# Performance work log

Measured on AMD Instinct MI355X. Metric: run time of the kernel, lower is better.

Reference implementation:

```python
import jax, jax.numpy as jnp
import numpy as np

B, L, D, H = 4, 4096, 2048, 128


def setup_inputs() -> dict:
    key = jax.random.key(0)
    k1, k2, k3, k4 = jax.random.split(key, 4)
    scale = 1.0 / np.sqrt(D)
    return {
        "x": jax.random.normal(k1, (B, L, D), dtype=jnp.float32),
        "Wq": jax.random.normal(k2, (D, H), dtype=jnp.float32) * scale,
        "Wk": jax.random.normal(k3, (D, H), dtype=jnp.float32) * scale,
        "Wv": jax.random.normal(k4, (D, H), dtype=jnp.float32) * scale,
    }


def reference(x, Wq, Wk, Wv):
    # single-head causal self-attention (dropout in eval mode / p=0)
    L_ = x.shape[1]
    q = jnp.einsum("bld,dh->blh", x, Wq)  # [B,L,H]
    k = jnp.einsum("bld,dh->blh", x, Wk)
    v = jnp.einsum("bld,dh->blh", x, Wv)
    scores = jnp.einsum("bqh,bkh->bqk", q, k) / jnp.sqrt(jnp.float32(q.shape[-1]))
    causal = jnp.tril(jnp.ones((L_, L_), dtype=bool))
    scores = jnp.where(causal, scores, -jnp.inf)
    probs = jax.nn.softmax(scores, axis=-1)
    return jnp.einsum("bqk,bkh->bqh", probs, v)
```

## Files before the change

kernel.cpp:

```cpp
#include <hip/hip_runtime.h>
#include <hip/hip_bf16.h>

#define B_ 4
#define L_ 4096
#define D_ 2048
#define H_ 128
#define M_ (B_ * L_)

typedef __attribute__((ext_vector_type(8))) short bf16x8;
typedef __attribute__((ext_vector_type(4))) float f32x4;
typedef __attribute__((ext_vector_type(16))) float f32x16;

__device__ __forceinline__ unsigned short f2bf(float f) {
  union { float f; unsigned u; } v; v.f = f;
  unsigned r = v.u + 0x7FFFu + ((v.u >> 16) & 1u);
  return (unsigned short)(r >> 16);
}

__device__ __forceinline__ unsigned cvt_pk_bf16(float lo, float hi) {
  unsigned r;
  asm("v_cvt_pk_bf16_f32 %0, %1, %2" : "=v"(r) : "v"(lo), "v"(hi));
  return r;
}

__device__ __forceinline__ void async_copy16(void* lds, const void* gptr) {
  __builtin_amdgcn_global_load_lds(
      (const __attribute__((address_space(1))) unsigned int*)gptr,
      (__attribute__((address_space(3))) unsigned int*)lds, 16, 0, 0);
}

__global__ void wconv(const float* __restrict__ Wq, const float* __restrict__ Wk,
                      const float* __restrict__ Wv, unsigned short* __restrict__ Wt) {
  int i = blockIdx.x * 256 + threadIdx.x;
  int m = i >> 18;
  int rem = i & 262143;
  int n = rem >> 11;
  int d = rem & 2047;
  const float* W = (m == 0) ? Wq : (m == 1 ? Wk : Wv);
  float val = W[(size_t)d * H_ + n];
  if (m == 0) val *= 0.08838834764831845f;
  int R = 96 * (n >> 5) + 32 * m + (n & 31);
  Wt[(size_t)R * D_ + d] = f2bf(val);
}

__global__ __launch_bounds__(512, 1) void qkv_gemm(
    const float* __restrict__ x, const unsigned short* __restrict__ Wt,
    unsigned short* __restrict__ qo, unsigned short* __restrict__ ko,
    unsigned short* __restrict__ vt) {
  __shared__ __align__(16) char Ab[2][16384];
  __shared__ __align__(16) char Bb[2][49152];

  int tid = threadIdx.x;
  int row0 = blockIdx.x * 64;
  int lane = tid & 63, w = tid >> 6;
  int wrow = (w >> 2) * 32;
  int g = w & 3;
  int l15 = lane & 15, lhi = lane >> 4;

  f32x4 zero = {0.f, 0.f, 0.f, 0.f};
  f32x4 acc[2][6];
#pragma unroll
  for (int i = 0; i < 2; i++)
#pragma unroll
    for (int j = 0; j < 6; j++) acc[i][j] = zero;

  const char* xg = (const char*)x;
  const char* wg = (const char*)Wt;

#pragma unroll
  for (int p = 0; p < 2; p++) {
    int o = (p * 512 + tid) * 16;
    int r = o >> 8;
    int cb = (o & 255) ^ ((r & 7) << 4);
    async_copy16(Ab[0] + o, xg + (((size_t)(row0 + r) * D_) << 2) + cb);
  }
#pragma unroll
  for (int p = 0; p < 6; p++) {
    int o = (p * 512 + tid) * 16;
    int r = o >> 7;
    int cb = (o & 127) ^ ((r & 7) << 4);
    async_copy16(Bb[0] + o, wg + (((size_t)r * D_) << 1) + cb);
  }
  __syncthreads();

  for (int t = 0; t < 32; t++) {
    int buf = t & 1;
    if (t < 31) {
      int k0 = (t + 1) * 64;
#pragma unroll
      for (int p = 0; p < 2; p++) {
        int o = (p * 512 + tid) * 16;
        int r = o >> 8;
        int cb = (o & 255) ^ ((r & 7) << 4);
        async_copy16(Ab[buf ^ 1] + o, xg + (((size_t)(row0 + r) * D_ + k0) << 2) + cb);
      }
#pragma unroll
      for (int p = 0; p < 6; p++) {
        int o = (p * 512 + tid) * 16;
        int r = o >> 7;
        int cb = (o & 127) ^ ((r & 7) << 4);
        async_copy16(Bb[buf ^ 1] + o, wg + (((size_t)r * D_ + k0) << 1) + cb);
      }
    }
    const char* A = Ab[buf];
    const char* Bp = Bb[buf];
#pragma unroll
    for (int ks = 0; ks < 2; ks++) {
      bf16x8 af[2], bfr[6];
#pragma unroll
      for (int mi = 0; mi < 2; mi++) {
        int r = wrow + mi * 16 + l15;
        int sw = (r & 7) << 4;
        int cb = ks * 128 + lhi * 32;
        float4 lo = *(const float4*)(A + r * 256 + (cb ^ sw));
        float4 hi = *(const float4*)(A + r * 256 + ((cb + 16) ^ sw));
        union { bf16x8 v; unsigned u[4]; } tt;
        tt.u[0] = cvt_pk_bf16(lo.x, lo.y);
        tt.u[1] = cvt_pk_bf16(lo.z, lo.w);
        tt.u[2] = cvt_pk_bf16(hi.x, hi.y);
        tt.u[3] = cvt_pk_bf16(hi.z, hi.w);
        af[mi] = tt.v;
      }
#pragma unroll
      for (int ni = 0; ni < 6; ni++) {
        int r = g * 96 + ni * 16 + l15;
        int sw = (r & 7) << 4;
        int cb = ks * 64 + lhi * 16;
        bfr[ni] = *(const bf16x8*)(Bp + r * 128 + (cb ^ sw));
      }
#pragma unroll
      for (int mi = 0; mi < 2; mi++)
#pragma unroll
        for (int ni = 0; ni < 6; ni++)
          acc[mi][ni] = __builtin_amdgcn_mfma_f32_16x16x32_bf16(af[mi], bfr[ni], acc[mi][ni], 0, 0, 0);
    }
    __syncthreads();
  }

#pragma unroll
  for (int ni = 0; ni < 4; ni++) {
    unsigned short* dst = (ni < 2) ? qo : ko;
    int nn = 32 * g + (ni & 1) * 16 + l15;
#pragma unroll
    for (int mi = 0; mi < 2; mi++)
#pragma unroll
      for (int r = 0; r < 4; r++) {
        int m = row0 + wrow + mi * 16 + lhi * 4 + r;
        dst[(size_t)m * H_ + nn] = f2bf(acc[mi][ni][r]);
      }
  }
  unsigned short* Tls = (unsigned short*)(Bb[0]) + w * 1280;
#pragma unroll
  for (int ni = 4; ni < 6; ni++)
#pragma unroll
    for (int mi = 0; mi < 2; mi++)
#pragma unroll
      for (int r = 0; r < 4; r++)
        Tls[((ni - 4) * 16 + l15) * 40 + mi * 16 + lhi * 4 + r] = f2bf(acc[mi][ni][r]);
  {
    int b = row0 >> 12;
    int Lbase = (row0 & 4095) + wrow;
    int n_loc = lane >> 1;
    int half = (lane & 1) * 16;
    int h = 32 * g + n_loc;
#pragma unroll
    for (int j = 0; j < 2; j++) {
      bf16x8 v = *(const bf16x8*)&Tls[n_loc * 40 + half + j * 8];
      *(bf16x8*)&vt[(((size_t)(b * H_ + h)) << 12) + Lbase + half + j * 8] = v;
    }
  }
}

__global__ __launch_bounds__(256, 2) void attn(
    const unsigned short* __restrict__ q, const unsigned short* __restrict__ k,
    const unsigned short* __restrict__ vt, float* __restrict__ po,
    float* __restrict__ pm, float* __restrict__ pl) {
  __shared__ __align__(16) char Kb[2][16384];
  __shared__ __align__(16) char Vb[2][16384];

  int bid = blockIdx.x;
  int b = bid & 3;
  int p2 = bid >> 2;
  int j, c;
  if (p2 < 32)      { j = 31 - (p2 >> 2);            c = p2 & 3; }
  else if (p2 < 56) { int i = p2 - 32; int d3 = i / 3; j = 23 - d3; c = i - 3 * d3; }
  else if (p2 < 72) { int i = p2 - 56; j = 15 - (i >> 1); c = i & 1; }
  else              { j = 7 - (p2 - 72);             c = 0; }

  int kbase = c << 10;
  int kmax = min((c + 1) << 10, (j + 1) << 7);
  int NT = (kmax - kbase) >> 6;

  int tid = threadIdx.x;
  int w = tid >> 6, lane = tid & 63;
  int q31 = lane & 31, hi = lane >> 5;
  int qw0 = (j << 7) + (w << 5);
  int kcap = qw0 + 32;

  const unsigned short* qb = q + ((size_t)b << 12) * H_;
  const char* kbyte = (const char*)(k + ((size_t)b << 12) * H_);
  const char* vbyte = (const char*)(vt + ((size_t)b * H_ << 12));

  bf16x8 qf[8];
#pragma unroll
  for (int kk = 0; kk < 8; kk++)
    qf[kk] = *(const bf16x8*)&qb[(size_t)(qw0 + q31) * H_ + kk * 16 + hi * 8];

  f32x16 o[4];
#pragma unroll
  for (int hb = 0; hb < 4; hb++)
#pragma unroll
    for (int r = 0; r < 16; r++) o[hb][r] = 0.f;
  float mrun = -1e30f, lrun = 0.f;

  int ksw = (q31 & 7) << 4;

#define STAGE(bi, k0)                                                          \
  {                                                                            \
    _Pragma("unroll") for (int p = 0; p < 4; p++) {                            \
      int oo = (p * 256 + tid) * 16;                                           \
      int rr = oo >> 8;                                                        \
      int cc = (oo & 255) ^ ((rr & 7) << 4);                                   \
      async_copy16(Kb[bi] + oo, kbyte + (size_t)((k0) + rr) * 256 + cc);       \
    }                                                                          \
    _Pragma("unroll") for (int p = 0; p < 4; p++) {                            \
      int oo = (p * 256 + tid) * 16;                                           \
      int hh = oo >> 7;                                                        \
      int cc = (oo & 127) ^ ((hh & 7) << 4);                                   \
      async_copy16(Vb[bi] + oo, vbyte + (size_t)hh * 8192 + (size_t)(k0) * 2 + cc); \
    }                                                                          \
  }

  STAGE(0, kbase);

  for (int t = 0; t < NT; t++) {
    __syncthreads();
    int k0 = kbase + (t << 6);
    if (t + 1 < NT) STAGE((t + 1) & 1, k0 + 64);
    const char* Kc = Kb[t & 1];
    const char* Vc = Vb[t & 1];

#pragma unroll
    for (int sub = 0; sub < 2; sub++) {
      int k0s = k0 + (sub << 5);
      if (k0s < kcap) {
        int kloc2 = sub << 5;
        const char* Krow = Kc + (kloc2 + q31) * 256;
        f32x16 s;
#pragma unroll
        for (int r = 0; r < 16; r++) s[r] = 0.f;
#pragma unroll
        for (int kk = 0; kk < 8; kk++) {
          bf16x8 kf = *(const bf16x8*)(Krow + ((kk * 32 + hi * 16) ^ ksw));
          s = __builtin_amdgcn_mfma_f32_32x32x16_bf16(kf, qf[kk], s, 0, 0, 0);
        }
        if (k0s == qw0) {
#pragma unroll
          for (int r = 0; r < 16; r++) {
            int kloc = (r & 3) + 8 * (r >> 2) + 4 * hi;
            if (kloc > q31) s[r] = -1e30f;
          }
        }
        float m0 = fmaxf(fmaxf(s[0], s[1]), fmaxf(s[2], s[3]));
        float m1 = fmaxf(fmaxf(s[4], s[5]), fmaxf(s[6], s[7]));
        float m2 = fmaxf(fmaxf(s[8], s[9]), fmaxf(s[10], s[11]));
        float m3 = fmaxf(fmaxf(s[12], s[13]), fmaxf(s[14], s[15]));
        float mt = fmaxf(fmaxf(m0, m1), fmaxf(m2, m3));
        mt = fmaxf(mt, __shfl_xor(mt, 32, 64));
        if (!__all(mt <= mrun + 8.f)) {
          float mn = fmaxf(mrun, mt);
          float al = __expf(mrun - mn);
          mrun = mn;
          lrun *= al;
#pragma unroll
          for (int hb = 0; hb < 4; hb++)
#pragma unroll
            for (int r = 0; r < 16; r++) o[hb][r] *= al;
        }
        float p[16], ls = 0.f;
#pragma unroll
        for (int r = 0; r < 16; r++) {
          p[r] = __expf(s[r] - mrun);
          ls += p[r];
        }
        ls += __shfl_xor(ls, 32, 64);
        lrun += ls;
        unsigned c0 = cvt_pk_bf16(p[0], p[1]),   c1 = cvt_pk_bf16(p[2], p[3]);
        unsigned c2 = cvt_pk_bf16(p[4], p[5]),   c3 = cvt_pk_bf16(p[6], p[7]);
        unsigned c4 = cvt_pk_bf16(p[8], p[9]),   c5 = cvt_pk_bf16(p[10], p[11]);
        unsigned c6 = cvt_pk_bf16(p[12], p[13]), c7 = cvt_pk_bf16(p[14], p[15]);
        unsigned e0 = (unsigned)__shfl_xor((int)(hi ? c0 : c2), 32, 64);
        unsigned e1 = (unsigned)__shfl_xor((int)(hi ? c1 : c3), 32, 64);
        unsigned e2 = (unsigned)__shfl_xor((int)(hi ? c4 : c6), 32, 64);
        unsigned e3 = (unsigned)__shfl_xor((int)(hi ? c5 : c7), 32, 64);
        union { unsigned u[4]; bf16x8 v; } pb0, pb1;
        pb0.u[0] = hi ? e0 : c0; pb0.u[1] = hi ? e1 : c1;
        pb0.u[2] = hi ? c2 : e0; pb0.u[3] = hi ? c3 : e1;
        pb1.u[0] = hi ? e2 : c4; pb1.u[1] = hi ? e3 : c5;
        pb1.u[2] = hi ? c6 : e2; pb1.u[3] = hi ? c7 : e3;
#pragma unroll
        for (int hb = 0; hb < 4; hb++) {
          const char* Vrow = Vc + (hb * 32 + q31) * 128;
          bf16x8 v0 = *(const bf16x8*)(Vrow + ((kloc2 * 2 + hi * 16) ^ ksw));
          bf16x8 v1 = *(const bf16x8*)(Vrow + ((kloc2 * 2 + 32 + hi * 16) ^ ksw));
          o[hb] = __builtin_amdgcn_mfma_f32_32x32x16_bf16(v0, pb0.v, o[hb], 0, 0, 0);
          o[hb] = __builtin_amdgcn_mfma_f32_32x32x16_bf16(v1, pb1.v, o[hb], 0, 0, 0);
        }
      }
    }
  }
#undef STAGE

  int qtile = (j << 2) + w;
  int slot = (((b << 7) + qtile) << 2) + c;
  float* pob = po + ((size_t)slot << 12);
#pragma unroll
  for (int hb = 0; hb < 4; hb++)
#pragma unroll
    for (int rq = 0; rq < 4; rq++) {
      float4 v;
      v.x = o[hb][rq * 4 + 0];
      v.y = o[hb][rq * 4 + 1];
      v.z = o[hb][rq * 4 + 2];
      v.w = o[hb][rq * 4 + 3];
      *(float4*)&pob[q31 * 128 + 32 * hb + 8 * rq + 4 * hi] = v;
    }
  if (lane < 32) {
    pm[slot * 32 + q31] = mrun;
    pl[slot * 32 + q31] = lrun;
  }
}

__global__ __launch_bounds__(256) void combine(
    const float* __restrict__ po, const float* __restrict__ pm,
    const float* __restrict__ pl, float* __restrict__ out) {
  int bid = blockIdx.x;
  int b = bid >> 7, t = bid & 127;
  int nc = (((t + 1) << 5) + 1023) >> 10;
  int tid = threadIdx.x;
  int row = tid >> 3;
  int hb = (tid & 7) << 4;
  int base = bid * 4;

  float M = -1e30f;
  for (int ci = 0; ci < nc; ci++) M = fmaxf(M, pm[(base + ci) * 32 + row]);
  float L = 0.f;
  float a[16];
#pragma unroll
  for (int j = 0; j < 16; j++) a[j] = 0.f;
  for (int ci = 0; ci < nc; ci++) {
    int sl = base + ci;
    float wgt = __expf(pm[sl * 32 + row] - M);
    L += pl[sl * 32 + row] * wgt;
    const float* p = po + ((size_t)sl << 12) + row * 128 + hb;
#pragma unroll
    for (int j = 0; j < 4; j++) {
      float4 v = *(const float4*)(p + j * 4);
      a[j * 4 + 0] += v.x * wgt;
      a[j * 4 + 1] += v.y * wgt;
      a[j * 4 + 2] += v.z * wgt;
      a[j * 4 + 3] += v.w * wgt;
    }
  }
  float inv = 1.f / L;
  float* ob = out + ((size_t)((b << 12) + (t << 5) + row)) * 128 + hb;
#pragma unroll
  for (int j = 0; j < 16; j++) ob[j] = a[j] * inv;
}

extern "C" void kernel_launch(void* const* d_in, const int* in_sizes, int n_in,
                              void* d_out, int out_size, void* d_ws, size_t ws_size,
                              hipStream_t stream) {
  const float* x  = (const float*)d_in[0];
  const float* Wq = (const float*)d_in[1];
  const float* Wk = (const float*)d_in[2];
  const float* Wv = (const float*)d_in[3];

  unsigned short* ws = (unsigned short*)d_ws;
  unsigned short* Wt = ws;
  unsigned short* qo = ws + 786432;
  unsigned short* ko = qo + (size_t)M_ * H_;
  unsigned short* vt = ko + (size_t)M_ * H_;
  float* po = (float*)(vt + (size_t)M_ * H_);
  float* pm = po + (size_t)2048 * 4096;
  float* pl = pm + 2048 * 32;
  float* out = (float*)d_out;

  hipLaunchKernelGGL(wconv, dim3(3072), dim3(256), 0, stream, Wq, Wk, Wv, Wt);
  hipLaunchKernelGGL(qkv_gemm, dim3(256), dim3(512), 0, stream, x, Wt, qo, ko, vt);
  hipLaunchKernelGGL(attn, dim3(320), dim3(256), 0, stream, qo, ko, vt, po, pm, pl);
  hipLaunchKernelGGL(combine, dim3(512), dim3(256), 0, stream, po, pm, pl, out);
}
```

Baseline: 286.9 us.

## Halve QKV GEMM k-tile to fit more blocks per CU with explicit vmcnt waits

The QKV projection GEMM's k-step shrinks from 64 to 32, halving its LDS double buffers, and launch bounds go from 1 to 4 blocks per CU so more workgroups can be resident. The __syncthreads at the top of each iteration becomes an explicit s_waitcnt vmcnt(4) plus s_barrier, so the next stage's async copies can stay in flight while the current buffer is consumed. The cost is twice as many iterations and barriers, smaller swizzle patterns, and register pressure under the tighter launch bound.

```diff
diff --git a/kernel.cpp b/kernel.cpp
--- a/kernel.cpp
+++ b/kernel.cpp
@@ -43,12 +43,12 @@
   Wt[(size_t)R * D_ + d] = f2bf(val);
 }
 
-__global__ __launch_bounds__(512, 1) void qkv_gemm(
+__global__ __launch_bounds__(512, 4) void qkv_gemm(
     const float* __restrict__ x, const unsigned short* __restrict__ Wt,
     unsigned short* __restrict__ qo, unsigned short* __restrict__ ko,
     unsigned short* __restrict__ vt) {
-  __shared__ __align__(16) char Ab[2][16384];
-  __shared__ __align__(16) char Bb[2][49152];
+  __shared__ __align__(16) char Ab[2][8192];
+  __shared__ __align__(16) char Bb[2][24576];
 
   int tid = threadIdx.x;
   int row0 = blockIdx.x * 64;
@@ -67,75 +67,68 @@
   const char* xg = (const char*)x;
   const char* wg = (const char*)Wt;
 
-#pragma unroll
-  for (int p = 0; p < 2; p++) {
-    int o = (p * 512 + tid) * 16;
-    int r = o >> 8;
-    int cb = (o & 255) ^ ((r & 7) << 4);
-    async_copy16(Ab[0] + o, xg + (((size_t)(row0 + r) * D_) << 2) + cb);
-  }
-#pragma unroll
-  for (int p = 0; p < 6; p++) {
-    int o = (p * 512 + tid) * 16;
-    int r = o >> 7;
-    int cb = (o & 127) ^ ((r & 7) << 4);
-    async_copy16(Bb[0] + o, wg + (((size_t)r * D_) << 1) + cb);
-  }
-  __syncthreads();
-
-  for (int t = 0; t < 32; t++) {
+#define QSTAGE(bi, k0)                                                         \
+  {                                                                            \
+    {                                                                          \
+      int o = tid * 16;                                                        \
+      int r = o >> 7;                                                          \
+      int cb = (o & 127) ^ ((r & 7) << 4);                                     \
+      async_copy16(Ab[bi] + o, xg + (((size_t)(row0 + r) * D_ + (k0)) << 2) + cb); \
+    }                                                                          \
+    _Pragma("unroll") for (int p = 0; p < 3; p++) {                            \
+      int o = (p * 512 + tid) * 16;                                            \
+      int r = o >> 6;                                                          \
+      int cb = (o & 63) ^ ((r & 3) << 4);                                      \
+      async_copy16(Bb[bi] + o, wg + (((size_t)r * D_ + (k0)) << 1) + cb);      \
+    }                                                                          \
+  }
+
+  QSTAGE(0, 0);
+
+  for (int t = 0; t < 64; t++) {
     int buf = t & 1;
-    if (t < 31) {
-      int k0 = (t + 1) * 64;
-#pragma unroll
-      for (int p = 0; p < 2; p++) {
-        int o = (p * 512 + tid) * 16;
-        int r = o >> 8;
-        int cb = (o & 255) ^ ((r & 7) << 4);
-        async_copy16(Ab[buf ^ 1] + o, xg + (((size_t)(row0 + r) * D_ + k0) << 2) + cb);
-      }
-#pragma unroll
-      for (int p = 0; p < 6; p++) {
-        int o = (p * 512 + tid) * 16;
-        int r = o >> 7;
-        int cb = (o & 127) ^ ((r & 7) << 4);
-        async_copy16(Bb[buf ^ 1] + o, wg + (((size_t)r * D_ + k0) << 1) + cb);
-      }
-    }
+    if (t < 63) {
+      QSTAGE(buf ^ 1, (t + 1) * 32);
+      asm volatile("s_waitcnt vmcnt(4)" ::: "memory");
+    } else {
+      asm volatile("s_waitcnt vmcnt(0)" ::: "memory");
+    }
+    __builtin_amdgcn_s_barrier();
+
     const char* A = Ab[buf];
     const char* Bp = Bb[buf];
-#pragma unroll
-    for (int ks = 0; ks < 2; ks++) {
-      bf16x8 af[2], bfr[6];
-#pragma unroll
-      for (int mi = 0; mi < 2; mi++) {
-        int r = wrow + mi * 16 + l15;
-        int sw = (r & 7) << 4;
-        int cb = ks * 128 + lhi * 32;
-        float4 lo = *(const float4*)(A + r * 256 + (cb ^ sw));
-        float4 hi = *(const float4*)(A + r * 256 + ((cb + 16) ^ sw));
-        union { bf16x8 v; unsigned u[4]; } tt;
-        tt.u[0] = cvt_pk_bf16(lo.x, lo.y);
-        tt.u[1] = cvt_pk_bf16(lo.z, lo.w);
-        tt.u[2] = cvt_pk_bf16(hi.x, hi.y);
-        tt.u[3] = cvt_pk_bf16(hi.z, hi.w);
-        af[mi] = tt.v;
-      }
-#pragma unroll
-      for (int ni = 0; ni < 6; ni++) {
-        int r = g * 96 + ni * 16 + l15;
-        int sw = (r & 7) << 4;
-        int cb = ks * 64 + lhi * 16;
-        bfr[ni] = *(const bf16x8*)(Bp + r * 128 + (cb ^ sw));
-      }
-#pragma unroll
-      for (int mi = 0; mi < 2; mi++)
-#pragma unroll
-        for (int ni = 0; ni < 6; ni++)
-          acc[mi][ni] = __builtin_amdgcn_mfma_f32_16x16x32_bf16(af[mi], bfr[ni], acc[mi][ni], 0, 0, 0);
-    }
-    __syncthreads();
-  }
+    bf16x8 af[2], bfr[6];
+#pragma unroll
+    for (int mi = 0; mi < 2; mi++) {
+      int r = wrow + mi * 16 + l15;
+      int sw = (r & 7) << 4;
+      int cb = lhi * 32;
+      float4 lo = *(const float4*)(A + r * 128 + (cb ^ sw));
+      float4 hi = *(const float4*)(A + r * 128 + ((cb + 16) ^ sw));
+      union { bf16x8 v; unsigned u[4]; } tt;
+      tt.u[0] = cvt_pk_bf16(lo.x, lo.y);
+      tt.u[1] = cvt_pk_bf16(lo.z, lo.w);
+      tt.u[2] = cvt_pk_bf16(hi.x, hi.y);
+      tt.u[3] = cvt_pk_bf16(hi.z, hi.w);
+      af[mi] = tt.v;
+    }
+#pragma unroll
+    for (int ni = 0; ni < 6; ni++) {
+      int r = g * 96 + ni * 16 + l15;
+      int sw = (r & 3) << 4;
+      int cb = lhi * 16;
+      bfr[ni] = *(const bf16x8*)(Bp + r * 64 + (cb ^ sw));
+    }
+#pragma unroll
+    for (int mi = 0; mi < 2; mi++)
+#pragma unroll
+      for (int ni = 0; ni < 6; ni++)
+        acc[mi][ni] = __builtin_amdgcn_mfma_f32_16x16x32_bf16(af[mi], bfr[ni], acc[mi][ni], 0, 0, 0);
+
+    asm volatile("" ::: "memory");
+    __builtin_amdgcn_s_barrier();
+  }
+#undef QSTAGE
 
 #pragma unroll
   for (int ni = 0; ni < 4; ni++) {
```

New measurement: 300.3 us. 4.7% more time.

## Split QKV GEMM per matrix into 768 smaller blocks with XCD-aware mapping

Applied to the files above, without the earlier changes.

The QKV projection used to run 256 blocks of 512 threads, each computing all 384 output columns for 64 rows. It now runs 768 blocks of 256 threads, each computing 128 columns of one matrix (Q, K or V), with a blockIdx mapping that groups row tiles by XCD. Occupancy goes up to 4 blocks per CU with single-buffered LDS. The cost is that the x tile (fp32) is re-read three times and the double-buffered async prefetch is gone, so load latency is no longer overlapped within a block.

```diff
diff --git a/kernel.cpp b/kernel.cpp
--- a/kernel.cpp
+++ b/kernel.cpp
@@ -39,81 +39,68 @@
   const float* W = (m == 0) ? Wq : (m == 1 ? Wk : Wv);
   float val = W[(size_t)d * H_ + n];
   if (m == 0) val *= 0.08838834764831845f;
-  int R = 96 * (n >> 5) + 32 * m + (n & 31);
-  Wt[(size_t)R * D_ + d] = f2bf(val);
-}
-
-__global__ __launch_bounds__(512, 1) void qkv_gemm(
+  Wt[(((size_t)(m << 7) + n) << 11) + d] = f2bf(val);
+}
+
+__global__ __launch_bounds__(256, 4) void qkv_gemm(
     const float* __restrict__ x, const unsigned short* __restrict__ Wt,
     unsigned short* __restrict__ qo, unsigned short* __restrict__ ko,
     unsigned short* __restrict__ vt) {
-  __shared__ __align__(16) char Ab[2][16384];
-  __shared__ __align__(16) char Bb[2][49152];
+  __shared__ __align__(16) char Sm[32768];
+  char* Ab = Sm;
+  char* Bb = Sm + 16384;
+
+  int bid = blockIdx.x;
+  int xcd = bid & 7;
+  int qq = bid >> 3;
+  int mat = qq % 3;
+  int rt = (qq / 3) * 8 + xcd;
+  int row0 = rt * 64;
 
   int tid = threadIdx.x;
-  int row0 = blockIdx.x * 64;
   int lane = tid & 63, w = tid >> 6;
-  int wrow = (w >> 2) * 32;
-  int g = w & 3;
+  int wrow = (w >> 1) * 32;
+  int wcol = (w & 1) * 64;
   int l15 = lane & 15, lhi = lane >> 4;
 
   f32x4 zero = {0.f, 0.f, 0.f, 0.f};
-  f32x4 acc[2][6];
+  f32x4 acc[2][4];
 #pragma unroll
   for (int i = 0; i < 2; i++)
 #pragma unroll
-    for (int j = 0; j < 6; j++) acc[i][j] = zero;
+    for (int j = 0; j < 4; j++) acc[i][j] = zero;
 
   const char* xg = (const char*)x;
-  const char* wg = (const char*)Wt;
-
-#pragma unroll
-  for (int p = 0; p < 2; p++) {
-    int o = (p * 512 + tid) * 16;
-    int r = o >> 8;
-    int cb = (o & 255) ^ ((r & 7) << 4);
-    async_copy16(Ab[0] + o, xg + (((size_t)(row0 + r) * D_) << 2) + cb);
-  }
-#pragma unroll
-  for (int p = 0; p < 6; p++) {
-    int o = (p * 512 + tid) * 16;
-    int r = o >> 7;
-    int cb = (o & 127) ^ ((r & 7) << 4);
-    async_copy16(Bb[0] + o, wg + (((size_t)r * D_) << 1) + cb);
-  }
-  __syncthreads();
+  const char* wg = (const char*)(Wt + ((size_t)mat << 7) * D_);
 
   for (int t = 0; t < 32; t++) {
-    int buf = t & 1;
-    if (t < 31) {
-      int k0 = (t + 1) * 64;
-#pragma unroll
-      for (int p = 0; p < 2; p++) {
-        int o = (p * 512 + tid) * 16;
-        int r = o >> 8;
-        int cb = (o & 255) ^ ((r & 7) << 4);
-        async_copy16(Ab[buf ^ 1] + o, xg + (((size_t)(row0 + r) * D_ + k0) << 2) + cb);
-      }
-#pragma unroll
-      for (int p = 0; p < 6; p++) {
-        int o = (p * 512 + tid) * 16;
-        int r = o >> 7;
-        int cb = (o & 127) ^ ((r & 7) << 4);
-        async_copy16(Bb[buf ^ 1] + o, wg + (((size_t)r * D_ + k0) << 1) + cb);
-      }
-    }
-    const char* A = Ab[buf];
-    const char* Bp = Bb[buf];
+    int k0 = t * 64;
+#pragma unroll
+    for (int p = 0; p < 4; p++) {
+      int o = (p * 256 + tid) * 16;
+      int r = o >> 8;
+      int cb = (o & 255) ^ ((r & 7) << 4);
+      async_copy16(Ab + o, xg + (((size_t)(row0 + r) * D_ + k0) << 2) + cb);
+    }
+#pragma unroll
+    for (int p = 0; p < 4; p++) {
+      int o = (p * 256 + tid) * 16;
+      int r = o >> 7;
+      int cb = (o & 127) ^ ((r & 7) << 4);
+      async_copy16(Bb + o, wg + (((size_t)r * D_ + k0) << 1) + cb);
+    }
+    __syncthreads();
+
 #pragma unroll
     for (int ks = 0; ks < 2; ks++) {
-      bf16x8 af[2], bfr[6];
+      bf16x8 af[2], bfr[4];
 #pragma unroll
       for (int mi = 0; mi < 2; mi++) {
         int r = wrow + mi * 16 + l15;
         int sw = (r & 7) << 4;
         int cb = ks * 128 + lhi * 32;
-        float4 lo = *(const float4*)(A + r * 256 + (cb ^ sw));
-        float4 hi = *(const float4*)(A + r * 256 + ((cb + 16) ^ sw));
+        float4 lo = *(const float4*)(Ab + r * 256 + (cb ^ sw));
+        float4 hi = *(const float4*)(Ab + r * 256 + ((cb + 16) ^ sw));
         union { bf16x8 v; unsigned u[4]; } tt;
         tt.u[0] = cvt_pk_bf16(lo.x, lo.y);
         tt.u[1] = cvt_pk_bf16(lo.z, lo.w);
@@ -122,51 +109,49 @@
         af[mi] = tt.v;
       }
 #pragma unroll
-      for (int ni = 0; ni < 6; ni++) {
-        int r = g * 96 + ni * 16 + l15;
+      for (int ni = 0; ni < 4; ni++) {
+        int r = wcol + ni * 16 + l15;
         int sw = (r & 7) << 4;
         int cb = ks * 64 + lhi * 16;
-        bfr[ni] = *(const bf16x8*)(Bp + r * 128 + (cb ^ sw));
+        bfr[ni] = *(const bf16x8*)(Bb + r * 128 + (cb ^ sw));
       }
 #pragma unroll
       for (int mi = 0; mi < 2; mi++)
 #pragma unroll
-        for (int ni = 0; ni < 6; ni++)
+        for (int ni = 0; ni < 4; ni++)
           acc[mi][ni] = __builtin_amdgcn_mfma_f32_16x16x32_bf16(af[mi], bfr[ni], acc[mi][ni], 0, 0, 0);
     }
     __syncthreads();
   }
 
-#pragma unroll
-  for (int ni = 0; ni < 4; ni++) {
-    unsigned short* dst = (ni < 2) ? qo : ko;
-    int nn = 32 * g + (ni & 1) * 16 + l15;
+  if (mat < 2) {
+    unsigned short* dst = (mat == 0) ? qo : ko;
 #pragma unroll
     for (int mi = 0; mi < 2; mi++)
 #pragma unroll
-      for (int r = 0; r < 4; r++) {
-        int m = row0 + wrow + mi * 16 + lhi * 4 + r;
-        dst[(size_t)m * H_ + nn] = f2bf(acc[mi][ni][r]);
-      }
-  }
-  unsigned short* Tls = (unsigned short*)(Bb[0]) + w * 1280;
-#pragma unroll
-  for (int ni = 4; ni < 6; ni++)
-#pragma unroll
-    for (int mi = 0; mi < 2; mi++)
-#pragma unroll
-      for (int r = 0; r < 4; r++)
-        Tls[((ni - 4) * 16 + l15) * 40 + mi * 16 + lhi * 4 + r] = f2bf(acc[mi][ni][r]);
-  {
+      for (int ni = 0; ni < 4; ni++)
+#pragma unroll
+        for (int r = 0; r < 4; r++) {
+          int m = row0 + wrow + mi * 16 + lhi * 4 + r;
+          int cc = wcol + ni * 16 + l15;
+          dst[(size_t)m * H_ + cc] = f2bf(acc[mi][ni][r]);
+        }
+  } else {
+    unsigned short* Tls = (unsigned short*)Sm + w * 2560;
+#pragma unroll
+    for (int ni = 0; ni < 4; ni++)
+#pragma unroll
+      for (int mi = 0; mi < 2; mi++)
+#pragma unroll
+        for (int r = 0; r < 4; r++)
+          Tls[(ni * 16 + l15) * 40 + mi * 16 + lhi * 4 + r] = f2bf(acc[mi][ni][r]);
     int b = row0 >> 12;
     int Lbase = (row0 & 4095) + wrow;
-    int n_loc = lane >> 1;
-    int half = (lane & 1) * 16;
-    int h = 32 * g + n_loc;
-#pragma unroll
-    for (int j = 0; j < 2; j++) {
-      bf16x8 v = *(const bf16x8*)&Tls[n_loc * 40 + half + j * 8];
-      *(bf16x8*)&vt[(((size_t)(b * H_ + h)) << 12) + Lbase + half + j * 8] = v;
+    int h = wcol + lane;
+#pragma unroll
+    for (int j = 0; j < 4; j++) {
+      bf16x8 v = *(const bf16x8*)&Tls[lane * 40 + j * 8];
+      *(bf16x8*)&vt[(((size_t)(b * H_ + h)) << 12) + Lbase + j * 8] = v;
     }
   }
 }
@@ -387,7 +372,7 @@
   float* out = (float*)d_out;
 
   hipLaunchKernelGGL(wconv, dim3(3072), dim3(256), 0, stream, Wq, Wk, Wv, Wt);
-  hipLaunchKernelGGL(qkv_gemm, dim3(256), dim3(512), 0, stream, x, Wt, qo, ko, vt);
+  hipLaunchKernelGGL(qkv_gemm, dim3(768), dim3(256), 0, stream, x, Wt, qo, ko, vt);
   hipLaunchKernelGGL(attn, dim3(320), dim3(256), 0, stream, qo, ko, vt, po, pm, pl);
   hipLaunchKernelGGL(combine, dim3(512), dim3(256), 0, stream, po, pm, pl, out);
 }
```

Result: no change. 281.4 us (-1.9%).
